# Performance work log

Measured on AMD Instinct MI355X. Metric: run time of the kernel, lower is better.

Reference implementation:

```python
import jax, jax.numpy as jnp
import numpy as np

EMBED_DIM = 256
NUM_CLASSES = 10


def setup_inputs() -> dict:
    key = jax.random.key(0)
    k1, k2, k3, k4 = jax.random.split(key, 4)
    x = jax.random.normal(k1, (64, 196, 768), dtype=jnp.float32)
    ag_w = jax.random.normal(k2, (EMBED_DIM, 768), dtype=jnp.float32)
    ag_b = jax.random.normal(k3, (EMBED_DIM,), dtype=jnp.float32)
    lm_w = jax.random.normal(k4, (EMBED_DIM * NUM_CLASSES, 768), dtype=jnp.float32)
    return {"x": x, "ag_w": ag_w, "ag_b": ag_b, "lm_w": lm_w}


def reference(x, ag_w, ag_b, lm_w):
    # x: (B, HW, D); ag_w: (E, D); ag_b: (E,); lm_w: (E*C, D)
    B, HW, D = x.shape
    E, C = EMBED_DIM, NUM_CLASSES
    # frozen arrangement generator -> binary sign pattern (B, HW, E)
    sign_patterns = (jnp.einsum('bhd,ed->bhe', x, ag_w) + ag_b > 0).astype(x.dtype)
    # linear map: (B, HW, E*C) -> (B, HW, E, C)
    z = jnp.einsum('bhd,pd->bhp', x, lm_w).reshape(B, HW, E, C)
    # masked reduction over HW and embed dims
    preds = jnp.einsum('bhp,bhpc->bc', sign_patterns, z) / HW
    return preds / E
```

## Files before the change

### kernel.cpp

```cpp
#include <hip/hip_runtime.h>

#define B_    64
#define HW_   196
#define HWP_  224
#define D_    768
#define E_    256
#define C_    10
#define MP_   (B_*HWP_)
#define K3K_  (E_*D_)
#define K3NB_ 256

typedef _Float16 f16x8 __attribute__((ext_vector_type(8)));
typedef _Float16 f16x4 __attribute__((ext_vector_type(4)));
typedef __bf16 bf16x8 __attribute__((ext_vector_type(8)));
typedef __bf16 bf16x4 __attribute__((ext_vector_type(4)));
typedef __bf16 bf16x2 __attribute__((ext_vector_type(2)));
typedef float  f32x4  __attribute__((ext_vector_type(4)));

__device__ __forceinline__ void gld_lds16(const void* g, void* l) {
  __builtin_amdgcn_global_load_lds((const __attribute__((address_space(1))) void*)g,
                                   (__attribute__((address_space(3))) void*)l, 16, 0, 0);
}

__global__ __launch_bounds__(256) void k0_prep(const float* __restrict__ w,
                                               _Float16* __restrict__ w16) {
  size_t i4 = ((size_t)blockIdx.x * 256 + threadIdx.x) * 4;
  float4 v = *(const float4*)&w[i4];
  f16x4 h;
  h[0] = (_Float16)v.x; h[1] = (_Float16)v.y;
  h[2] = (_Float16)v.z; h[3] = (_Float16)v.w;
  *(f16x4*)&w16[i4] = h;
}

__global__ __launch_bounds__(256) void k1_signs(const float* __restrict__ x,
                                                const _Float16* __restrict__ w16,
                                                const float* __restrict__ bias,
                                                __bf16* __restrict__ st) {
  __shared__ __align__(16) char smem[59392];
  const int m0 = blockIdx.x * 64;
  const int tid = threadIdx.x;
  const int wave = tid >> 6, lane = tid & 63;
  const int wn = wave * 64;
  const int q = lane >> 4, l15 = lane & 15;
  const int swq = (q ^ ((l15 >> 1) & 3)) * 8;

  const int ar = tid >> 2, ac = (tid & 3) * 8;
  const int am = m0 + ar;
  const int ab = am / HWP_;
  const int ahp = am - ab * HWP_;
  const bool avalid = (ahp < HW_);
  const float* aptr = &x[((size_t)ab * HW_ + (avalid ? ahp : 0)) * D_ + ac];

  const int swB = ((tid & 3) ^ ((tid >> 3) & 3)) * 8;
  const size_t offB = (size_t)(tid >> 2) * D_ + swB;

  f32x4 acc[4][4] = {};
  float4 aX0, aX1, aY0, aY1;

#define K1_LOADA(r0, r1, kk) do { \
    r0 = *(const float4*)&aptr[(kk)]; \
    r1 = *(const float4*)&aptr[(kk) + 4]; \
  } while (0)

#define K1_CONV(bufA, r0, r1) do { \
    _Float16* AW = (_Float16*)(smem + 49152 + (bufA) * 5120); \
    float va[8] = {r0.x, r0.y, r0.z, r0.w, r1.x, r1.y, r1.z, r1.w}; \
    f16x8 hh; \
    _Pragma("unroll") \
    for (int j = 0; j < 8; j++) { \
      float vj = avalid ? va[j] : 0.0f; \
      hh[j] = (_Float16)vj; \
    } \
    *(f16x8*)&AW[ar * 40 + ac] = hh; \
  } while (0)

#define K1_DMAB(buf3, kk) do { \
    char* bb = smem + (buf3) * 16384; \
    _Pragma("unroll") \
    for (int c = 0; c < 4; c++) { \
      gld_lds16(&w16[offB + (size_t)c * 64 * D_ + (kk)], bb + c * 4096 + wave * 1024); \
    } \
  } while (0)

#define K1_COMPUTE(buf3, bufA) do { \
    const _Float16* BL = (const _Float16*)(smem + (buf3) * 16384); \
    const _Float16* AL = (const _Float16*)(smem + 49152 + (bufA) * 5120); \
    f16x8 ah[4], bh[4]; \
    _Pragma("unroll") \
    for (int t = 0; t < 4; t++) { \
      ah[t] = *(const f16x8*)&AL[(t * 16 + l15) * 40 + q * 8]; \
      bh[t] = *(const f16x8*)&BL[(wn + t * 16 + l15) * 32 + swq]; \
    } \
    __builtin_amdgcn_s_setprio(1); \
    _Pragma("unroll") \
    for (int mt = 0; mt < 4; mt++) \
      _Pragma("unroll") \
      for (int nt = 0; nt < 4; nt++) \
        acc[mt][nt] = __builtin_amdgcn_mfma_f32_16x16x32_f16(ah[mt], bh[nt], acc[mt][nt], 0, 0, 0); \
    __builtin_amdgcn_s_setprio(0); \
  } while (0)

#define K1_BAR() do { \
    asm volatile("s_waitcnt lgkmcnt(0)" ::: "memory"); \
    __builtin_amdgcn_s_barrier(); \
    __builtin_amdgcn_sched_barrier(0); \
  } while (0)

  K1_DMAB(0, 0);
  __builtin_amdgcn_sched_barrier(0);
  K1_LOADA(aX0, aX1, 0);
  __builtin_amdgcn_sched_barrier(0);
  K1_DMAB(1, 32);
  __builtin_amdgcn_sched_barrier(0);
  K1_LOADA(aY0, aY1, 32);
  K1_CONV(0, aX0, aX1);
  K1_BAR();

#pragma unroll
  for (int t = 0; t < 22; ++t) {
    K1_DMAB((t + 2) % 3, (t + 2) * 32);
    __builtin_amdgcn_sched_barrier(0);
    if ((t & 1) == 0) K1_LOADA(aX0, aX1, (t + 2) * 32);
    else              K1_LOADA(aY0, aY1, (t + 2) * 32);
    K1_COMPUTE(t % 3, t & 1);
    if ((t & 1) == 0) K1_CONV(1, aY0, aY1);
    else              K1_CONV(0, aX0, aX1);
    K1_BAR();
  }
  K1_COMPUTE(22 % 3, 0);
  K1_CONV(1, aY0, aY1);
  K1_BAR();
  K1_COMPUTE(23 % 3, 1);
  K1_BAR();

#undef K1_LOADA
#undef K1_CONV
#undef K1_DMAB
#undef K1_COMPUTE
#undef K1_BAR

  __bf16* Sload = (__bf16*)smem;
#pragma unroll
  for (int mt = 0; mt < 4; mt++)
#pragma unroll
    for (int nt = 0; nt < 4; nt++) {
      int e = wn + nt * 16 + l15;
      float bv = bias[e];
      bf16x4 o;
#pragma unroll
      for (int r = 0; r < 4; r++) {
        int m = m0 + mt * 16 + q * 4 + r;
        int b = m / HWP_;
        int hp = m - b * HWP_;
        float v = acc[mt][nt][r] + bv;
        o[r] = (hp < HW_ && v > 0.0f) ? (__bf16)1.0f : (__bf16)0.0f;
      }
      *(bf16x4*)&Sload[e * 72 + mt * 16 + q * 4] = o;
    }
  __syncthreads();
#pragma unroll
  for (int it = 0; it < 16; it++) {
    int e = (tid >> 4) + it * 16;
    int m4 = (tid & 15) * 4;
    bf16x4 v = *(const bf16x4*)&Sload[e * 72 + m4];
    int mabs = m0 + m4;
    int b = mabs / HWP_;
    int hp = mabs - b * HWP_;
    *(bf16x4*)&st[((size_t)b * E_ + e) * HWP_ + hp] = v;
  }
}

__global__ __launch_bounds__(512) void k2_g(const __bf16* __restrict__ st,
                                            const float* __restrict__ x,
                                            __bf16* __restrict__ g) {
  __shared__ __align__(16) __bf16 As[2][256 * 32];
  __shared__ __align__(16) __bf16 Bs[2][128 * 40];
  const int f = blockIdx.x;
  const int xcd = f & 7;
  const int slot = f >> 3;
  const int b  = xcd + 8 * (slot / 6);
  const int d0 = (slot % 6) * 128;
  const int tid = threadIdx.x;
  const int wave = tid >> 6, lane = tid & 63;
  const int WE = (wave & 3) * 64;
  const int WD = (wave >> 2) * 64;
  const int q = lane >> 4, l15 = lane & 15;
  const int ar = tid >> 2, ac = (tid & 3) * 8;
  const int ldA = wave * 512;
  const int dg = tid & 31, kp = tid >> 5;
  f32x4 acc[4][4] = {};

  const __bf16* gA = &st[((size_t)b * E_ + ar) * HWP_ + ac];
  const float4 zero4 = make_float4(0.f, 0.f, 0.f, 0.f);
  float4 f0, f1;

#define K2_STAGEA(buf, kk) do { \
    gld_lds16(gA + (kk),                       &As[buf][ldA]); \
    gld_lds16(gA + (size_t)128 * HWP_ + (kk),  &As[buf][4096 + ldA]); \
  } while (0)

#define K2_LOADB(kk) do { \
    int hp0 = (kk) + 2 * kp; \
    const float* bsrc = &x[((size_t)b * HW_ + hp0) * D_ + d0 + 4 * dg]; \
    f0 = (hp0     < HW_) ? *(const float4*)&bsrc[0]  : zero4; \
    f1 = (hp0 + 1 < HW_) ? *(const float4*)&bsrc[D_] : zero4; \
  } while (0)

#define K2_WRITEB(buf) do { \
    float rr0[4] = {f0.x, f0.y, f0.z, f0.w}; \
    float rr1[4] = {f1.x, f1.y, f1.z, f1.w}; \
    _Pragma("unroll") \
    for (int j = 0; j < 4; j++) { \
      bf16x2 o; \
      o[0] = (__bf16)rr0[j]; o[1] = (__bf16)rr1[j]; \
      *(bf16x2*)&Bs[buf][(4 * dg + j) * 40 + 2 * kp] = o; \
    } \
  } while (0)

  K2_STAGEA(0, 0);
  K2_LOADB(0);
  K2_WRITEB(0);
  __syncthreads();

  int cur = 0;
  for (int k0 = 0; k0 < HWP_; k0 += 32) {
    const bool have = (k0 + 32 < HWP_);
    if (have) {
      K2_STAGEA(cur ^ 1, k0 + 32);
      K2_LOADB(k0 + 32);
    }
    bf16x8 af[4], bfr[4];
#pragma unroll
    for (int t = 0; t < 4; t++) {
      af[t]  = *(const bf16x8*)&As[cur][(WE + t * 16 + l15) * 32 + q * 8];
      bfr[t] = *(const bf16x8*)&Bs[cur][(WD + t * 16 + l15) * 40 + q * 8];
    }
#pragma unroll
    for (int mt = 0; mt < 4; mt++)
#pragma unroll
      for (int nt = 0; nt < 4; nt++)
        acc[mt][nt] = __builtin_amdgcn_mfma_f32_16x16x32_bf16(af[mt], bfr[nt], acc[mt][nt], 0, 0, 0);
    if (have) K2_WRITEB(cur ^ 1);
    __syncthreads();
    cur ^= 1;
  }
#undef K2_STAGEA
#undef K2_LOADB
#undef K2_WRITEB

#pragma unroll
  for (int mt = 0; mt < 4; mt++)
#pragma unroll
    for (int nt = 0; nt < 4; nt++) {
      int d = d0 + WD + nt * 16 + l15;
#pragma unroll
      for (int r = 0; r < 4; r++) {
        int e = WE + mt * 16 + q * 4 + r;
        g[((size_t)b * E_ + e) * D_ + d] = (__bf16)acc[mt][nt][r];
      }
    }
}

__global__ __launch_bounds__(256) void k3_mfma(const __bf16* __restrict__ g,
                                               const float* __restrict__ lmw,
                                               float* __restrict__ part) {
  __shared__ float sp[B_ * C_];
  const int tid = threadIdx.x;
  const int wave = tid >> 6, lane = tid & 63;
  const int q = lane >> 4, l15 = lane & 15;
  const int e = blockIdx.x;
  f32x4 acc[4] = {};

  for (int i = tid; i < B_ * C_; i += 256) sp[i] = 0.0f;

#pragma unroll
  for (int ks = 0; ks < 6; ks++) {
    int d = wave * 192 + ks * 32 + q * 8;
    size_t k = (size_t)e * D_ + d;
    bf16x8 bfrag;
    if (l15 < C_) {
      const float* bp = &lmw[((size_t)e * C_ + l15) * D_ + d];
      float4 b0 = *(const float4*)&bp[0];
      float4 b1 = *(const float4*)&bp[4];
      float bb[8] = {b0.x, b0.y, b0.z, b0.w, b1.x, b1.y, b1.z, b1.w};
#pragma unroll
      for (int j = 0; j < 8; j++) bfrag[j] = (__bf16)bb[j];
    } else {
#pragma unroll
      for (int j = 0; j < 8; j++) bfrag[j] = (__bf16)0.0f;
    }
#pragma unroll
    for (int mt = 0; mt < 4; mt++) {
      bf16x8 afrag = *(const bf16x8*)&g[(size_t)(mt * 16 + l15) * K3K_ + k];
      acc[mt] = __builtin_amdgcn_mfma_f32_16x16x32_bf16(afrag, bfrag, acc[mt], 0, 0, 0);
    }
  }
  __syncthreads();
  if (l15 < C_) {
#pragma unroll
    for (int mt = 0; mt < 4; mt++)
#pragma unroll
      for (int r = 0; r < 4; r++) {
        int b = mt * 16 + q * 4 + r;
        atomicAdd(&sp[b * C_ + l15], acc[mt][r]);
      }
  }
  __syncthreads();
  for (int i = tid; i < B_ * C_; i += 256)
    part[(size_t)blockIdx.x * (B_ * C_) + i] = sp[i];
}

__global__ __launch_bounds__(256) void k4_reduce(const float* __restrict__ part,
                                                 float* __restrict__ out) {
  __shared__ float sp[256];
  const int b = blockIdx.x;
  const int tid = threadIdx.x;
  const int c = tid & 15, g16 = tid >> 4;
  float s = 0.0f;
  if (c < C_) {
#pragma unroll
    for (int j = 0; j < 16; j++)
      s += part[(size_t)(g16 + 16 * j) * (B_ * C_) + b * C_ + c];
  }
  sp[tid] = s;
  __syncthreads();
  if (tid < C_) {
    float t = 0.0f;
#pragma unroll
    for (int j = 0; j < 16; j++) t += sp[j * 16 + tid];
    out[b * C_ + tid] = t * (1.0f / (196.0f * 256.0f));
  }
}

extern "C" void kernel_launch(void* const* d_in, const int* in_sizes, int n_in,
                              void* d_out, int out_size, void* d_ws, size_t ws_size,
                              hipStream_t stream) {
  const float* x    = (const float*)d_in[0];
  const float* ag_w = (const float*)d_in[1];
  const float* ag_b = (const float*)d_in[2];
  const float* lm_w = (const float*)d_in[3];
  float* out = (float*)d_out;

  char* ws = (char*)d_ws;
  const size_t W_BYTES  = (size_t)E_ * D_ * 2;
  const size_t ST_BYTES = (size_t)B_ * E_ * HWP_ * 2;
  const size_t G_BYTES  = (size_t)B_ * E_ * D_ * 2;
  _Float16* w16 = (_Float16*)(ws);
  __bf16* st    = (__bf16*)(ws + W_BYTES);
  __bf16* gb    = (__bf16*)(ws + W_BYTES + ST_BYTES);
  float*  part  = (float*)(ws + W_BYTES + ST_BYTES + G_BYTES);

  k0_prep<<<dim3((E_ * D_) / 4 / 256), dim3(256), 0, stream>>>(ag_w, w16);
  k1_signs<<<dim3(MP_ / 64), dim3(256), 0, stream>>>(x, w16, ag_b, st);
  k2_g<<<dim3(6 * B_), dim3(512), 0, stream>>>(st, x, gb);
  k3_mfma<<<dim3(K3NB_), dim3(256), 0, stream>>>(gb, lm_w, part);
  k4_reduce<<<dim3(B_), dim3(256), 0, stream>>>(part, out);
}
```

Baseline: 143.1 us.

## Switch intermediates to fp16 and split k2/k3 work across more blocks and waves

Changes the sign-pattern and g intermediates and the MFMA ops from bf16 to fp16. k2 is split so each block covers half of the E dimension with 256 threads, which doubles the grid to 768 blocks, and each thread now loads four HW rows of x instead of two. k3 moves to 512 threads with half the K steps per wave. The aim is more parallelism and better occupancy in the two GEMM stages, at the cost of x being reloaded once per E-half in k2 and a possible fp16 range or precision issue for g.

```diff
diff --git a/kernel.cpp b/kernel.cpp
--- a/kernel.cpp
+++ b/kernel.cpp
@@ -12,9 +12,7 @@
 
 typedef _Float16 f16x8 __attribute__((ext_vector_type(8)));
 typedef _Float16 f16x4 __attribute__((ext_vector_type(4)));
-typedef __bf16 bf16x8 __attribute__((ext_vector_type(8)));
-typedef __bf16 bf16x4 __attribute__((ext_vector_type(4)));
-typedef __bf16 bf16x2 __attribute__((ext_vector_type(2)));
+typedef _Float16 f16x2 __attribute__((ext_vector_type(2)));
 typedef float  f32x4  __attribute__((ext_vector_type(4)));
 
 __device__ __forceinline__ void gld_lds16(const void* g, void* l) {
@@ -35,7 +33,7 @@
 __global__ __launch_bounds__(256) void k1_signs(const float* __restrict__ x,
                                                 const _Float16* __restrict__ w16,
                                                 const float* __restrict__ bias,
-                                                __bf16* __restrict__ st) {
+                                                _Float16* __restrict__ st) {
   __shared__ __align__(16) char smem[59392];
   const int m0 = blockIdx.x * 64;
   const int tid = threadIdx.x;
@@ -139,81 +137,88 @@
 #undef K1_COMPUTE
 #undef K1_BAR
 
-  __bf16* Sload = (__bf16*)smem;
+  _Float16* Sload = (_Float16*)smem;
 #pragma unroll
   for (int mt = 0; mt < 4; mt++)
 #pragma unroll
     for (int nt = 0; nt < 4; nt++) {
       int e = wn + nt * 16 + l15;
       float bv = bias[e];
-      bf16x4 o;
+      f16x4 o;
 #pragma unroll
       for (int r = 0; r < 4; r++) {
         int m = m0 + mt * 16 + q * 4 + r;
         int b = m / HWP_;
         int hp = m - b * HWP_;
         float v = acc[mt][nt][r] + bv;
-        o[r] = (hp < HW_ && v > 0.0f) ? (__bf16)1.0f : (__bf16)0.0f;
+        o[r] = (hp < HW_ && v > 0.0f) ? (_Float16)1.0f : (_Float16)0.0f;
       }
-      *(bf16x4*)&Sload[e * 72 + mt * 16 + q * 4] = o;
+      *(f16x4*)&Sload[e * 72 + mt * 16 + q * 4] = o;
     }
   __syncthreads();
 #pragma unroll
   for (int it = 0; it < 16; it++) {
     int e = (tid >> 4) + it * 16;
     int m4 = (tid & 15) * 4;
-    bf16x4 v = *(const bf16x4*)&Sload[e * 72 + m4];
+    f16x4 v = *(const f16x4*)&Sload[e * 72 + m4];
     int mabs = m0 + m4;
     int b = mabs / HWP_;
     int hp = mabs - b * HWP_;
-    *(bf16x4*)&st[((size_t)b * E_ + e) * HWP_ + hp] = v;
-  }
-}
-
-__global__ __launch_bounds__(512) void k2_g(const __bf16* __restrict__ st,
+    *(f16x4*)&st[((size_t)b * E_ + e) * HWP_ + hp] = v;
+  }
+}
+
+__global__ __launch_bounds__(256) void k2_g(const _Float16* __restrict__ st,
                                             const float* __restrict__ x,
-                                            __bf16* __restrict__ g) {
-  __shared__ __align__(16) __bf16 As[2][256 * 32];
-  __shared__ __align__(16) __bf16 Bs[2][128 * 40];
+                                            _Float16* __restrict__ g) {
+  __shared__ __align__(16) _Float16 As[2][128 * 32];
+  __shared__ __align__(16) _Float16 Bs[2][128 * 40];
   const int f = blockIdx.x;
   const int xcd = f & 7;
-  const int slot = f >> 3;
-  const int b  = xcd + 8 * (slot / 6);
-  const int d0 = (slot % 6) * 128;
+  const int s = f >> 3;
+  const int b  = xcd + 8 * (s / 12);
+  const int r12 = s % 12;
+  const int eh = r12 / 6;
+  const int d0 = (r12 % 6) * 128;
   const int tid = threadIdx.x;
   const int wave = tid >> 6, lane = tid & 63;
-  const int WE = (wave & 3) * 64;
-  const int WD = (wave >> 2) * 64;
+  const int WEl = (wave & 1) * 64;
+  const int WD  = (wave >> 1) * 64;
   const int q = lane >> 4, l15 = lane & 15;
   const int ar = tid >> 2, ac = (tid & 3) * 8;
   const int ldA = wave * 512;
   const int dg = tid & 31, kp = tid >> 5;
   f32x4 acc[4][4] = {};
 
-  const __bf16* gA = &st[((size_t)b * E_ + ar) * HWP_ + ac];
+  const _Float16* gA = &st[((size_t)b * E_ + eh * 128 + ar) * HWP_ + ac];
   const float4 zero4 = make_float4(0.f, 0.f, 0.f, 0.f);
-  float4 f0, f1;
+  float4 f0, f1, f2, f3;
 
 #define K2_STAGEA(buf, kk) do { \
-    gld_lds16(gA + (kk),                       &As[buf][ldA]); \
-    gld_lds16(gA + (size_t)128 * HWP_ + (kk),  &As[buf][4096 + ldA]); \
+    gld_lds16(gA + (kk),                      &As[buf][ldA]); \
+    gld_lds16(gA + (size_t)64 * HWP_ + (kk),  &As[buf][2048 + ldA]); \
   } while (0)
 
 #define K2_LOADB(kk) do { \
-    int hp0 = (kk) + 2 * kp; \
+    int hp0 = (kk) + 4 * kp; \
     const float* bsrc = &x[((size_t)b * HW_ + hp0) * D_ + d0 + 4 * dg]; \
-    f0 = (hp0     < HW_) ? *(const float4*)&bsrc[0]  : zero4; \
-    f1 = (hp0 + 1 < HW_) ? *(const float4*)&bsrc[D_] : zero4; \
+    f0 = (hp0     < HW_) ? *(const float4*)&bsrc[0]      : zero4; \
+    f1 = (hp0 + 1 < HW_) ? *(const float4*)&bsrc[D_]     : zero4; \
+    f2 = (hp0 + 2 < HW_) ? *(const float4*)&bsrc[2 * D_] : zero4; \
+    f3 = (hp0 + 3 < HW_) ? *(const float4*)&bsrc[3 * D_] : zero4; \
   } while (0)
 
 #define K2_WRITEB(buf) do { \
     float rr0[4] = {f0.x, f0.y, f0.z, f0.w}; \
     float rr1[4] = {f1.x, f1.y, f1.z, f1.w}; \
+    float rr2[4] = {f2.x, f2.y, f2.z, f2.w}; \
+    float rr3[4] = {f3.x, f3.y, f3.z, f3.w}; \
     _Pragma("unroll") \
     for (int j = 0; j < 4; j++) { \
-      bf16x2 o; \
-      o[0] = (__bf16)rr0[j]; o[1] = (__bf16)rr1[j]; \
-      *(bf16x2*)&Bs[buf][(4 * dg + j) * 40 + 2 * kp] = o; \
+      f16x4 o; \
+      o[0] = (_Float16)rr0[j]; o[1] = (_Float16)rr1[j]; \
+      o[2] = (_Float16)rr2[j]; o[3] = (_Float16)rr3[j]; \
+      *(f16x4*)&Bs[buf][(4 * dg + j) * 40 + 4 * kp] = o; \
     } \
   } while (0)
 
@@ -229,17 +234,17 @@
       K2_STAGEA(cur ^ 1, k0 + 32);
       K2_LOADB(k0 + 32);
     }
-    bf16x8 af[4], bfr[4];
+    f16x8 af[4], bfr[4];
 #pragma unroll
     for (int t = 0; t < 4; t++) {
-      af[t]  = *(const bf16x8*)&As[cur][(WE + t * 16 + l15) * 32 + q * 8];
-      bfr[t] = *(const bf16x8*)&Bs[cur][(WD + t * 16 + l15) * 40 + q * 8];
+      af[t]  = *(const f16x8*)&As[cur][(WEl + t * 16 + l15) * 32 + q * 8];
+      bfr[t] = *(const f16x8*)&Bs[cur][(WD + t * 16 + l15) * 40 + q * 8];
     }
 #pragma unroll
     for (int mt = 0; mt < 4; mt++)
 #pragma unroll
       for (int nt = 0; nt < 4; nt++)
-        acc[mt][nt] = __builtin_amdgcn_mfma_f32_16x16x32_bf16(af[mt], bfr[nt], acc[mt][nt], 0, 0, 0);
+        acc[mt][nt] = __builtin_amdgcn_mfma_f32_16x16x32_f16(af[mt], bfr[nt], acc[mt][nt], 0, 0, 0);
     if (have) K2_WRITEB(cur ^ 1);
     __syncthreads();
     cur ^= 1;
@@ -255,13 +260,13 @@
       int d = d0 + WD + nt * 16 + l15;
 #pragma unroll
       for (int r = 0; r < 4; r++) {
-        int e = WE + mt * 16 + q * 4 + r;
-        g[((size_t)b * E_ + e) * D_ + d] = (__bf16)acc[mt][nt][r];
+        int e = eh * 128 + WEl + mt * 16 + q * 4 + r;
+        g[((size_t)b * E_ + e) * D_ + d] = (_Float16)acc[mt][nt][r];
       }
     }
 }
 
-__global__ __launch_bounds__(256) void k3_mfma(const __bf16* __restrict__ g,
+__global__ __launch_bounds__(512) void k3_mfma(const _Float16* __restrict__ g,
                                                const float* __restrict__ lmw,
                                                float* __restrict__ part) {
   __shared__ float sp[B_ * C_];
@@ -271,28 +276,28 @@
   const int e = blockIdx.x;
   f32x4 acc[4] = {};
 
-  for (int i = tid; i < B_ * C_; i += 256) sp[i] = 0.0f;
-
-#pragma unroll
-  for (int ks = 0; ks < 6; ks++) {
-    int d = wave * 192 + ks * 32 + q * 8;
+  for (int i = tid; i < B_ * C_; i += 512) sp[i] = 0.0f;
+
+#pragma unroll
+  for (int ks = 0; ks < 3; ks++) {
+    int d = wave * 96 + ks * 32 + q * 8;
     size_t k = (size_t)e * D_ + d;
-    bf16x8 bfrag;
+    f16x8 bfrag;
     if (l15 < C_) {
       const float* bp = &lmw[((size_t)e * C_ + l15) * D_ + d];
       float4 b0 = *(const float4*)&bp[0];
       float4 b1 = *(const float4*)&bp[4];
       float bb[8] = {b0.x, b0.y, b0.z, b0.w, b1.x, b1.y, b1.z, b1.w};
 #pragma unroll
-      for (int j = 0; j < 8; j++) bfrag[j] = (__bf16)bb[j];
+      for (int j = 0; j < 8; j++) bfrag[j] = (_Float16)bb[j];
     } else {
 #pragma unroll
-      for (int j = 0; j < 8; j++) bfrag[j] = (__bf16)0.0f;
+      for (int j = 0; j < 8; j++) bfrag[j] = (_Float16)0.0f;
     }
 #pragma unroll
     for (int mt = 0; mt < 4; mt++) {
-      bf16x8 afrag = *(const bf16x8*)&g[(size_t)(mt * 16 + l15) * K3K_ + k];
-      acc[mt] = __builtin_amdgcn_mfma_f32_16x16x32_bf16(afrag, bfrag, acc[mt], 0, 0, 0);
+      f16x8 afrag = *(const f16x8*)&g[(size_t)(mt * 16 + l15) * K3K_ + k];
+      acc[mt] = __builtin_amdgcn_mfma_f32_16x16x32_f16(afrag, bfrag, acc[mt], 0, 0, 0);
     }
   }
   __syncthreads();
@@ -306,7 +311,7 @@
       }
   }
   __syncthreads();
-  for (int i = tid; i < B_ * C_; i += 256)
+  for (int i = tid; i < B_ * C_; i += 512)
     part[(size_t)blockIdx.x * (B_ * C_) + i] = sp[i];
 }
 
@@ -346,13 +351,13 @@
   const size_t ST_BYTES = (size_t)B_ * E_ * HWP_ * 2;
   const size_t G_BYTES  = (size_t)B_ * E_ * D_ * 2;
   _Float16* w16 = (_Float16*)(ws);
-  __bf16* st    = (__bf16*)(ws + W_BYTES);
-  __bf16* gb    = (__bf16*)(ws + W_BYTES + ST_BYTES);
+  _Float16* st  = (_Float16*)(ws + W_BYTES);
+  _Float16* gb  = (_Float16*)(ws + W_BYTES + ST_BYTES);
   float*  part  = (float*)(ws + W_BYTES + ST_BYTES + G_BYTES);
 
   k0_prep<<<dim3((E_ * D_) / 4 / 256), dim3(256), 0, stream>>>(ag_w, w16);
   k1_signs<<<dim3(MP_ / 64), dim3(256), 0, stream>>>(x, w16, ag_b, st);
-  k2_g<<<dim3(6 * B_), dim3(512), 0, stream>>>(st, x, gb);
-  k3_mfma<<<dim3(K3NB_), dim3(256), 0, stream>>>(gb, lm_w, part);
+  k2_g<<<dim3(12 * B_), dim3(256), 0, stream>>>(st, x, gb);
+  k3_mfma<<<dim3(K3NB_), dim3(512), 0, stream>>>(gb, lm_w, part);
   k4_reduce<<<dim3(B_), dim3(256), 0, stream>>>(part, out);
 }
```

Measured after the change: 143.2 us. No clear change (+0.1%).
